# Kernel optimization log

Hardware: AMD Instinct MI355X
Metric: run time of the kernel (lower is better)

## Reference

```python
import jax, jax.numpy as jnp
import numpy as np

EPS = 1e-05

def setup_inputs() -> dict:
    key = jax.random.key(0)
    k1, k2, k3 = jax.random.split(key, 3)
    B, S, D_IN, D_OUT = 4, 2048, 4096, 12288
    x = jax.random.normal(k1, (B, S, D_IN), dtype=jnp.float32)
    weight = jax.random.normal(k2, (D_OUT, D_IN), dtype=jnp.float32) * (1.0 / np.sqrt(D_IN))
    bias = jnp.zeros((D_OUT,), dtype=jnp.float32)
    ln_weight = jnp.ones((D_IN,), dtype=jnp.float32)
    ln_bias = jnp.zeros((D_IN,), dtype=jnp.float32)
    return {"x": x, "weight": weight, "bias": bias, "ln_weight": ln_weight, "ln_bias": ln_bias}

def reference(x, weight, bias, ln_weight, ln_bias):
    # LayerNorm over last dim
    mean = jnp.mean(x, axis=-1, keepdims=True)
    var = jnp.mean(jnp.square(x - mean), axis=-1, keepdims=True)
    normed = (x - mean) * jax.lax.rsqrt(var + EPS) * ln_weight + ln_bias
    # Linear: y = normed @ W^T + b
    return jnp.einsum('bsd,od->bso', normed, weight) + bias
```

## Files before the change

kernel.cpp:

```cpp
#include <hip/hip_runtime.h>
#include <hip/hip_bf16.h>
#include <stdint.h>

typedef __attribute__((ext_vector_type(8))) short short8_t;
typedef __attribute__((ext_vector_type(4))) float f32x4;

__device__ __forceinline__ unsigned short f2bf(float f) {
  union { float f; unsigned int u; } a;
  a.f = f;
  unsigned int u = a.u;
  u += 0x7fffu + ((u >> 16) & 1u);
  return (unsigned short)(u >> 16);
}

__device__ __forceinline__ void gload_lds16(const void* g, void* l) {
  __builtin_amdgcn_global_load_lds(
      (const __attribute__((address_space(1))) void*)g,
      (__attribute__((address_space(3))) void*)l, 16, 0, 0);
}

constexpr int D_IN = 4096;

__global__ __launch_bounds__(256) void ln_bf16_kernel(
    const float* __restrict__ x, const float* __restrict__ lnw,
    const float* __restrict__ lnb, unsigned short* __restrict__ out) {
  const int row = blockIdx.x;
  const int tid = threadIdx.x;
  const float* xr = x + (size_t)row * D_IN;

  f32x4 v[4];
  float sum = 0.f, sq = 0.f;
#pragma unroll
  for (int i = 0; i < 4; ++i) {
    v[i] = __builtin_nontemporal_load(
        reinterpret_cast<const f32x4*>(xr + i * 1024 + tid * 4));
    sum += v[i][0] + v[i][1] + v[i][2] + v[i][3];
    sq += v[i][0]*v[i][0] + v[i][1]*v[i][1] + v[i][2]*v[i][2] + v[i][3]*v[i][3];
  }
#pragma unroll
  for (int off = 32; off > 0; off >>= 1) {
    sum += __shfl_down(sum, off, 64);
    sq  += __shfl_down(sq, off, 64);
  }
  __shared__ float s_sum[4], s_sq[4];
  if ((tid & 63) == 0) { s_sum[tid >> 6] = sum; s_sq[tid >> 6] = sq; }
  __syncthreads();
  const float fs = s_sum[0] + s_sum[1] + s_sum[2] + s_sum[3];
  const float fq = s_sq[0] + s_sq[1] + s_sq[2] + s_sq[3];
  const float mean = fs * (1.f / D_IN);
  const float var = fq * (1.f / D_IN) - mean * mean;
  const float rstd = rsqrtf(var + 1e-5f);

  unsigned short* orow = out + (size_t)row * D_IN;
#pragma unroll
  for (int i = 0; i < 4; ++i) {
    const int col = i * 1024 + tid * 4;
    const f32x4 w = *reinterpret_cast<const f32x4*>(lnw + col);
    const f32x4 b = *reinterpret_cast<const f32x4*>(lnb + col);
    ushort4 o;
    o.x = f2bf((v[i][0] - mean) * rstd * w[0] + b[0]);
    o.y = f2bf((v[i][1] - mean) * rstd * w[1] + b[1]);
    o.z = f2bf((v[i][2] - mean) * rstd * w[2] + b[2]);
    o.w = f2bf((v[i][3] - mean) * rstd * w[3] + b[3]);
    *reinterpret_cast<ushort4*>(orow + col) = o;
  }
}

__global__ __launch_bounds__(256) void f32_to_bf16_kernel(
    const float* __restrict__ in, unsigned short* __restrict__ out) {
  const size_t i = ((size_t)blockIdx.x * 256 + threadIdx.x) * 8;
  const f32x4 a = __builtin_nontemporal_load(reinterpret_cast<const f32x4*>(in + i));
  const f32x4 b = __builtin_nontemporal_load(reinterpret_cast<const f32x4*>(in + i + 4));
  ushort4 lo, hi;
  lo.x = f2bf(a[0]); lo.y = f2bf(a[1]); lo.z = f2bf(a[2]); lo.w = f2bf(a[3]);
  hi.x = f2bf(b[0]); hi.y = f2bf(b[1]); hi.z = f2bf(b[2]); hi.w = f2bf(b[3]);
  *reinterpret_cast<ushort4*>(out + i) = lo;
  *reinterpret_cast<ushort4*>(out + i + 4) = hi;
}


#define RDA(S, KK, ROW) \
  (*reinterpret_cast<const short8_t*>(((KK) ? aB1 : aB0) + (S)*32768 + (ROW)*128))
#define RDB(S, KK, ROW) \
  (*reinterpret_cast<const short8_t*>(((KK) ? bB1 : bB0) + (S)*32768 + (ROW)*128))

#define READ_A(S, MH)                                          \
  _Pragma("unroll") for (int m_ = 0; m_ < 4; ++m_) {           \
    af[m_][0] = RDA(S, 0, (MH)*64 + m_*16);                    \
    af[m_][1] = RDA(S, 1, (MH)*64 + m_*16);                    \
  }

#define READ_B(S, NH)                                          \
  _Pragma("unroll") for (int n_ = 0; n_ < 2; ++n_) {           \
    bfr[(NH)*2+n_][0] = RDB(S, 0, ((NH)*2+n_)*16);             \
    bfr[(NH)*2+n_][1] = RDB(S, 1, ((NH)*2+n_)*16);             \
  }

#define MFMA_Q(MH, NH)                                                         \
  _Pragma("unroll") for (int kk_ = 0; kk_ < 2; ++kk_) {                        \
    _Pragma("unroll") for (int m_ = 0; m_ < 4; ++m_) {                         \
      _Pragma("unroll") for (int n_ = 0; n_ < 2; ++n_)                         \
        acc[(MH)*4+m_][(NH)*2+n_] = __builtin_amdgcn_mfma_f32_16x16x32_bf16(   \
            af[m_][kk_], bfr[(NH)*2+n_][kk_], acc[(MH)*4+m_][(NH)*2+n_], 0, 0, 0); \
    }                                                                          \
  }

#define STAGE_A(S, U, KT) \
  gload_lds16(aSrc + (size_t)((U)*64) * K + (size_t)(KT)*64, ldsAw + (S)*32768 + (U)*8192)
#define STAGE_B(S, U, KT) \
  gload_lds16(bSrc + (size_t)((U)*64) * K + (size_t)(KT)*64, ldsBw + (S)*32768 + (U)*8192)

#define PH_MID                                         \
  __builtin_amdgcn_s_barrier();                        \
  __builtin_amdgcn_s_setprio(1)
#define PH_END                                         \
  __builtin_amdgcn_s_setprio(0);                       \
  asm volatile("s_waitcnt lgkmcnt(0)" ::: "memory");   \
  __builtin_amdgcn_s_barrier();                        \
  asm volatile("" ::: "memory")
#define PH_END_V(N)                                    \
  __builtin_amdgcn_s_setprio(0);                       \
  asm volatile("s_waitcnt lgkmcnt(0)\n\ts_waitcnt vmcnt(" #N ")" ::: "memory");\
  __builtin_amdgcn_s_barrier();                        \
  asm volatile("" ::: "memory")

__global__ __launch_bounds__(512, 2) void gemm_8phase(
    const unsigned short* __restrict__ A,
    const unsigned short* __restrict__ B,
    const float* __restrict__ bias,
    float* __restrict__ C,
    int M, int N, int K, int NYB, int BXP) {
  extern __shared__ char smem[];
  const int tid = threadIdx.x;
  const int lane = tid & 63;
  const int wid = tid >> 6;
  const int wr = wid >> 2, wc = wid & 3;
  const int fr = lane & 15;
  const int q16 = (lane >> 4) * 16;
  const int wr128 = wr * 128;
  const int wc64 = wc * 64;

  const int id = blockIdx.x;
  const int xcd = id & 7;
  const int slot = id >> 3;
  const int by = slot % NYB;
  const int bx = xcd * BXP + slot / NYB;
  const int m0 = by * 256, n0 = bx * 256;

  const int s_log = (tid * 16) ^ (((tid >> 3) & 7) << 4);
  const int rsw = s_log >> 7;
  const int csw = (s_log & 127) >> 1;
  const unsigned short* aSrc = A + (size_t)(m0 + rsw) * K + csw;
  const unsigned short* bSrc = B + (size_t)(n0 + rsw) * K + csw;

  char* const ldsAw = smem + wid * 1024;
  char* const ldsBw = smem + 65536 + wid * 1024;

  const int s7 = (fr & 7) << 4;
  const char* const aB0 = smem + (wr128 + fr) * 128 + (q16 ^ s7);
  const char* const aB1 = smem + (wr128 + fr) * 128 + ((64 + q16) ^ s7);
  const char* const bB0 = smem + 65536 + (wc64 + fr) * 128 + (q16 ^ s7);
  const char* const bB1 = smem + 65536 + (wc64 + fr) * 128 + ((64 + q16) ^ s7);

  f32x4 acc[8][4] = {};
  short8_t af[4][2], bfr[4][2];

  STAGE_A(0,0,0); STAGE_A(0,1,0); STAGE_A(0,2,0); STAGE_A(0,3,0);
  STAGE_B(0,0,0); STAGE_B(0,1,0); STAGE_B(0,2,0); STAGE_B(0,3,0);
  STAGE_A(1,0,1); STAGE_A(1,1,1); STAGE_A(1,2,1); STAGE_A(1,3,1);
  STAGE_B(1,0,1); STAGE_B(1,1,1);
  asm volatile("s_waitcnt vmcnt(6)" ::: "memory");
  __builtin_amdgcn_s_barrier();
  asm volatile("" ::: "memory");

  const int NT = K >> 7;
  for (int t = 0; t < NT - 1; ++t) {
    const int k1 = 2*t + 1, k2 = 2*t + 2, k3 = 2*t + 3;
    READ_A(0, 0) READ_B(0, 0)
    STAGE_B(1,2,k1); STAGE_B(1,3,k1);
    PH_MID; MFMA_Q(0,0) PH_END;
    READ_B(0, 1)
    STAGE_A(0,0,k2); STAGE_A(0,2,k2);
    PH_MID; MFMA_Q(0,1) PH_END;
    READ_A(0, 1)
    STAGE_B(0,0,k2); STAGE_B(0,1,k2);
    PH_MID; MFMA_Q(1,0) PH_END;
    STAGE_A(0,1,k2); STAGE_A(0,3,k2);
    PH_MID; MFMA_Q(1,1) PH_END_V(6);
    READ_A(1, 0) READ_B(1, 0)
    STAGE_B(0,2,k2); STAGE_B(0,3,k2);
    PH_MID; MFMA_Q(0,0) PH_END;
    READ_B(1, 1)
    STAGE_A(1,0,k3); STAGE_A(1,2,k3);
    PH_MID; MFMA_Q(0,1) PH_END;
    READ_A(1, 1)
    STAGE_B(1,0,k3); STAGE_B(1,1,k3);
    PH_MID; MFMA_Q(1,0) PH_END;
    STAGE_A(1,1,k3); STAGE_A(1,3,k3);
    PH_MID; MFMA_Q(1,1) PH_END_V(6);
  }
  {
    const int k1 = 2*NT - 1;
    READ_A(0, 0) READ_B(0, 0)
    STAGE_B(1,2,k1); STAGE_B(1,3,k1);
    PH_MID; MFMA_Q(0,0) PH_END;
    READ_B(0, 1)
    PH_MID; MFMA_Q(0,1) PH_END;
    READ_A(0, 1)
    PH_MID; MFMA_Q(1,0) PH_END;
    PH_MID; MFMA_Q(1,1) PH_END_V(0);
    READ_A(1, 0) READ_B(1, 0)
    PH_MID; MFMA_Q(0,0) PH_END;
    READ_B(1, 1)
    PH_MID; MFMA_Q(0,1) PH_END;
    READ_A(1, 1)
    PH_MID; MFMA_Q(1,0) PH_END;
    PH_MID; MFMA_Q(1,1)
    __builtin_amdgcn_s_setprio(0);
  }

  __syncthreads();
  float* const buf0 = (float*)smem;
  float* const buf1 = (float*)smem + 64 * 260;
  const int cr = (lane >> 4) * 4;
  float bv[4];
#pragma unroll
  for (int ni = 0; ni < 4; ++ni) bv[ni] = bias[n0 + wc64 + ni * 16 + fr];

#pragma unroll
  for (int half = 0; half < 2; ++half) {
    float* const wbuf = (wr == 0) ? buf0 : buf1;
#pragma unroll
    for (int mi4 = 0; mi4 < 4; ++mi4) {
      const int mi = half * 4 + mi4;
#pragma unroll
      for (int j = 0; j < 4; ++j) {
        const int lr = mi4 * 16 + cr + j;
#pragma unroll
        for (int ni = 0; ni < 4; ++ni)
          wbuf[lr * 260 + wc64 + ni * 16 + fr] = acc[mi][ni][j] + bv[ni];
      }
    }
    __syncthreads();
#pragma unroll
    for (int i = 0; i < 16; ++i) {
      const int idx = wid * 16 + i;
      const float* src = (idx < 64 ? buf0 + idx * 260 : buf1 + (idx - 64) * 260) + lane * 4;
      const int grow = m0 + (idx < 64 ? half * 64 + idx : 128 + half * 64 + (idx - 64));
      const f32x4 vv = *reinterpret_cast<const f32x4*>(src);
      __builtin_nontemporal_store(
          vv, reinterpret_cast<f32x4*>(C + (size_t)grow * N + n0) + lane);
    }
    __syncthreads();
  }
}

extern "C" void kernel_launch(void* const* d_in, const int* in_sizes, int n_in,
                              void* d_out, int out_size, void* d_ws, size_t ws_size,
                              hipStream_t stream) {
  const float* x    = (const float*)d_in[0];
  const float* w    = (const float*)d_in[1];
  const float* bias = (const float*)d_in[2];
  const float* lnw  = (const float*)d_in[3];
  const float* lnb  = (const float*)d_in[4];
  float* out = (float*)d_out;

  const int DIN  = 4096;
  const int M    = in_sizes[0] / DIN;
  const int DOUT = in_sizes[2];

  unsigned short* normA = (unsigned short*)d_ws;
  unsigned short* wB    = normA + (size_t)M * DIN;

  ln_bf16_kernel<<<M, 256, 0, stream>>>(x, lnw, lnb, normA);
  f32_to_bf16_kernel<<<((size_t)DOUT * DIN) / (256 * 8), 256, 0, stream>>>(w, wB);

  const int nwg = (M / 256) * (DOUT / 256);
  const int smem_bytes = 2 * 64 * 260 * 4 > 131072 ? 2 * 64 * 260 * 4 : 131072;
  (void)hipFuncSetAttribute((const void*)gemm_8phase,
                            hipFuncAttributeMaxDynamicSharedMemorySize, 163840);
  gemm_8phase<<<nwg, 512, smem_bytes, stream>>>(normA, wB, bias, out,
                                                M, DOUT, DIN, M / 256, (DOUT / 256) / 8);
}
```

Baseline: 769.7 us.

## Replace 8-phase GEMM schedule with two-region X/Y pipeline per K tile

Restructures the GEMM main loop so each 64-wide K tile is handled in two regions instead of four barrier-separated phases. The X region reads LDS fragments and runs the first half of the MFMAs. The Y region issues all global-to-LDS stages for a future tile, then runs the remaining MFMAs. This cuts the barriers per K tile from four to two and batches the async loads, aiming to lower synchronization overhead. In exchange there is less interleaving of loads with compute and a more bursty memory issue pattern.

```diff
diff --git a/kernel.cpp b/kernel.cpp
--- a/kernel.cpp
+++ b/kernel.cpp
@@ -109,22 +109,33 @@
   gload_lds16(aSrc + (size_t)((U)*64) * K + (size_t)(KT)*64, ldsAw + (S)*32768 + (U)*8192)
 #define STAGE_B(S, U, KT) \
   gload_lds16(bSrc + (size_t)((U)*64) * K + (size_t)(KT)*64, ldsBw + (S)*32768 + (U)*8192)
-
-#define PH_MID                                         \
-  __builtin_amdgcn_s_barrier();                        \
-  __builtin_amdgcn_s_setprio(1)
-#define PH_END                                         \
-  __builtin_amdgcn_s_setprio(0);                       \
-  asm volatile("s_waitcnt lgkmcnt(0)" ::: "memory");   \
-  __builtin_amdgcn_s_barrier();                        \
-  asm volatile("" ::: "memory")
-#define PH_END_V(N)                                    \
-  __builtin_amdgcn_s_setprio(0);                       \
-  asm volatile("s_waitcnt lgkmcnt(0)\n\ts_waitcnt vmcnt(" #N ")" ::: "memory");\
-  __builtin_amdgcn_s_barrier();                        \
-  asm volatile("" ::: "memory")
-
-__global__ __launch_bounds__(512, 2) void gemm_8phase(
+#define STAGE_ALL(S, KT)                                       \
+  STAGE_A(S,0,KT); STAGE_A(S,1,KT); STAGE_A(S,2,KT); STAGE_A(S,3,KT); \
+  STAGE_B(S,0,KT); STAGE_B(S,1,KT); STAGE_B(S,2,KT); STAGE_B(S,3,KT);
+
+#define XREG(S)                                                \
+  READ_A(S, 0) READ_B(S, 0)                                    \
+  __builtin_amdgcn_s_setprio(1);                               \
+  MFMA_Q(0,0)                                                  \
+  READ_B(S, 1)                                                 \
+  MFMA_Q(0,1)                                                  \
+  READ_A(S, 1)                                                 \
+  __builtin_amdgcn_s_setprio(0);                               \
+  asm volatile("s_waitcnt lgkmcnt(0)" ::: "memory");           \
+  __builtin_amdgcn_s_barrier();                                \
+  asm volatile("" ::: "memory");
+
+#define YREG(S, KT)                                            \
+  STAGE_ALL(S, KT)                                             \
+  __builtin_amdgcn_s_setprio(1);                               \
+  MFMA_Q(1,0)                                                  \
+  MFMA_Q(1,1)                                                  \
+  __builtin_amdgcn_s_setprio(0);                               \
+  asm volatile("s_waitcnt vmcnt(8)" ::: "memory");             \
+  __builtin_amdgcn_s_barrier();                                \
+  asm volatile("" ::: "memory");
+
+__global__ __launch_bounds__(512, 2) void gemm_xy(
     const unsigned short* __restrict__ A,
     const unsigned short* __restrict__ B,
     const float* __restrict__ bias,
@@ -165,57 +176,39 @@
   f32x4 acc[8][4] = {};
   short8_t af[4][2], bfr[4][2];
 
-  STAGE_A(0,0,0); STAGE_A(0,1,0); STAGE_A(0,2,0); STAGE_A(0,3,0);
-  STAGE_B(0,0,0); STAGE_B(0,1,0); STAGE_B(0,2,0); STAGE_B(0,3,0);
-  STAGE_A(1,0,1); STAGE_A(1,1,1); STAGE_A(1,2,1); STAGE_A(1,3,1);
-  STAGE_B(1,0,1); STAGE_B(1,1,1);
-  asm volatile("s_waitcnt vmcnt(6)" ::: "memory");
+  STAGE_ALL(0, 0)
+  STAGE_ALL(1, 1)
+  asm volatile("s_waitcnt vmcnt(8)" ::: "memory");
   __builtin_amdgcn_s_barrier();
   asm volatile("" ::: "memory");
 
-  const int NT = K >> 7;
-  for (int t = 0; t < NT - 1; ++t) {
-    const int k1 = 2*t + 1, k2 = 2*t + 2, k3 = 2*t + 3;
+  const int NK = K >> 6;
+  for (int t = 0; t < (NK - 2) >> 1; ++t) {
+    const int k2 = 2*t + 2, k3 = 2*t + 3;
+    XREG(0) YREG(0, k2)
+    XREG(1) YREG(1, k3)
+  }
+  {
     READ_A(0, 0) READ_B(0, 0)
-    STAGE_B(1,2,k1); STAGE_B(1,3,k1);
-    PH_MID; MFMA_Q(0,0) PH_END;
+    __builtin_amdgcn_s_setprio(1);
+    MFMA_Q(0,0)
     READ_B(0, 1)
-    STAGE_A(0,0,k2); STAGE_A(0,2,k2);
-    PH_MID; MFMA_Q(0,1) PH_END;
+    MFMA_Q(0,1)
     READ_A(0, 1)
-    STAGE_B(0,0,k2); STAGE_B(0,1,k2);
-    PH_MID; MFMA_Q(1,0) PH_END;
-    STAGE_A(0,1,k2); STAGE_A(0,3,k2);
-    PH_MID; MFMA_Q(1,1) PH_END_V(6);
+    MFMA_Q(1,0)
+    MFMA_Q(1,1)
+    __builtin_amdgcn_s_setprio(0);
+    asm volatile("s_waitcnt lgkmcnt(0)\n\ts_waitcnt vmcnt(0)" ::: "memory");
+    __builtin_amdgcn_s_barrier();
+    asm volatile("" ::: "memory");
     READ_A(1, 0) READ_B(1, 0)
-    STAGE_B(0,2,k2); STAGE_B(0,3,k2);
-    PH_MID; MFMA_Q(0,0) PH_END;
+    __builtin_amdgcn_s_setprio(1);
+    MFMA_Q(0,0)
     READ_B(1, 1)
-    STAGE_A(1,0,k3); STAGE_A(1,2,k3);
-    PH_MID; MFMA_Q(0,1) PH_END;
+    MFMA_Q(0,1)
     READ_A(1, 1)
-    STAGE_B(1,0,k3); STAGE_B(1,1,k3);
-    PH_MID; MFMA_Q(1,0) PH_END;
-    STAGE_A(1,1,k3); STAGE_A(1,3,k3);
-    PH_MID; MFMA_Q(1,1) PH_END_V(6);
-  }
-  {
-    const int k1 = 2*NT - 1;
-    READ_A(0, 0) READ_B(0, 0)
-    STAGE_B(1,2,k1); STAGE_B(1,3,k1);
-    PH_MID; MFMA_Q(0,0) PH_END;
-    READ_B(0, 1)
-    PH_MID; MFMA_Q(0,1) PH_END;
-    READ_A(0, 1)
-    PH_MID; MFMA_Q(1,0) PH_END;
-    PH_MID; MFMA_Q(1,1) PH_END_V(0);
-    READ_A(1, 0) READ_B(1, 0)
-    PH_MID; MFMA_Q(0,0) PH_END;
-    READ_B(1, 1)
-    PH_MID; MFMA_Q(0,1) PH_END;
-    READ_A(1, 1)
-    PH_MID; MFMA_Q(1,0) PH_END;
-    PH_MID; MFMA_Q(1,1)
+    MFMA_Q(1,0)
+    MFMA_Q(1,1)
     __builtin_amdgcn_s_setprio(0);
   }
 
@@ -277,8 +270,8 @@
 
   const int nwg = (M / 256) * (DOUT / 256);
   const int smem_bytes = 2 * 64 * 260 * 4 > 131072 ? 2 * 64 * 260 * 4 : 131072;
-  (void)hipFuncSetAttribute((const void*)gemm_8phase,
+  (void)hipFuncSetAttribute((const void*)gemm_xy,
                             hipFuncAttributeMaxDynamicSharedMemorySize, 163840);
-  gemm_8phase<<<nwg, 512, smem_bytes, stream>>>(normA, wB, bias, out,
-                                                M, DOUT, DIN, M / 256, (DOUT / 256) / 8);
-}
+  gemm_xy<<<nwg, 512, smem_bytes, stream>>>(normA, wB, bias, out,
+                                            M, DOUT, DIN, M / 256, (DOUT / 256) / 8);
+}
```

Measured after the change: 770.0 us. Within noise of the previous version (+0.0%).
